# Performance work log

Hardware: AMD Instinct MI355X
Metric: run time of the kernel (lower is better)

Reference implementation:

```python
import jax, jax.numpy as jnp
import numpy as np


def _affine_mats(thetas, lambda1s, lambda2s, H, W):
    # Replicates torch.stack(rows, dim=1) then stack(dim=2): the 'rows' end up as COLUMNS,
    # exactly matching the original module's construction.
    z = jnp.zeros_like(lambda1s)
    o = jnp.ones_like(lambda1s)
    scale = jnp.stack([jnp.stack([lambda1s, z, z], 1),
                       jnp.stack([z, lambda2s, z], 1),
                       jnp.stack([z, z, o], 1)], axis=2)  # [B,3,3]
    th = -thetas
    rot = jnp.stack([jnp.stack([jnp.cos(th), jnp.sin(th), z], 1),
                     jnp.stack([-jnp.sin(th), jnp.cos(th), z], 1),
                     jnp.stack([z, z, o], 1)], axis=2)
    trans = jnp.stack([jnp.stack([o, z, o * W], 1),
                       jnp.stack([z, o, o * H], 1),
                       jnp.stack([z, z, o], 1)], axis=2)
    fw = rot @ trans                       # forward_warp
    fws = scale @ fw                       # forward_warp_scaled
    overall = jnp.linalg.inv(jnp.linalg.inv(fw) @ fws)
    return overall[:, 0:2, :]              # [B,2,3]


def _affine_grid(theta, H, W):
    # torch affine_grid, align_corners=False: normalized pixel-center coords in [-1,1]
    xs = (jnp.arange(W, dtype=theta.dtype) + 0.5) * (2.0 / W) - 1.0
    ys = (jnp.arange(H, dtype=theta.dtype) + 0.5) * (2.0 / H) - 1.0
    X, Y = jnp.meshgrid(xs, ys)                        # [H,W]
    base = jnp.stack([X, Y, jnp.ones_like(X)], -1)     # [H,W,3]
    return jnp.einsum('bij,hwj->bhwi', theta, base)    # [B,H,W,2] (x,y)


def _grid_sample_bilinear_zeros(x, grid):
    # torch grid_sample(mode='bilinear', padding_mode='zeros', align_corners=False)
    B, C, H, W = x.shape
    gx = (grid[..., 0] + 1.0) * (W * 0.5) - 0.5        # [B,H,W] source pixel coords
    gy = (grid[..., 1] + 1.0) * (H * 0.5) - 0.5
    x0 = jnp.floor(gx); y0 = jnp.floor(gy)
    x1 = x0 + 1.0;      y1 = y0 + 1.0
    wx1 = gx - x0; wx0 = 1.0 - wx1
    wy1 = gy - y0; wy0 = 1.0 - wy1
    x0i = x0.astype(jnp.int32); x1i = x1.astype(jnp.int32)
    y0i = y0.astype(jnp.int32); y1i = y1.astype(jnp.int32)
    b_idx = jnp.arange(B)[:, None, None]

    def gather(yi, xi):
        yc = jnp.clip(yi, 0, H - 1)
        xc = jnp.clip(xi, 0, W - 1)
        v = x[b_idx, :, yc, xc]                        # [B,H,W,C]
        m = ((yi >= 0) & (yi < H) & (xi >= 0) & (xi < W)).astype(x.dtype)
        return v * m[..., None]

    out = (gather(y0i, x0i) * (wy0 * wx0)[..., None]
           + gather(y0i, x1i) * (wy0 * wx1)[..., None]
           + gather(y1i, x0i) * (wy1 * wx0)[..., None]
           + gather(y1i, x1i) * (wy1 * wx1)[..., None])  # [B,H,W,C]
    return jnp.transpose(out, (0, 3, 1, 2))            # [B,C,H,W]


def setup_inputs() -> dict:
    key = jax.random.key(0)
    k1, k2, k3, k4 = jax.random.split(key, 4)
    B, C, H, W = 32, 3, 512, 512
    return {
        'x': jax.random.normal(k1, (B, C, H, W), dtype=jnp.float32),
        'thetas': jax.random.normal(k2, (B,), dtype=jnp.float32),
        'lambda1s': jax.random.uniform(k3, (B,), dtype=jnp.float32),
        'lambda2s': jax.random.uniform(k4, (B,), dtype=jnp.float32),
    }


def reference(x, thetas, lambda1s, lambda2s):
    H, W = x.shape[2], x.shape[3]
    theta = _affine_mats(thetas, lambda1s, lambda2s, H, W)   # [B,2,3]
    grid = _affine_grid(theta, H, W)                         # [B,H,W,2]
    return _grid_sample_bilinear_zeros(x, grid).astype(jnp.float32)
```

## Files before the change

### kernel.cpp

```cpp
#include <hip/hip_runtime.h>
#include <math.h>

constexpr int B = 32;
constexpr int C = 3;
constexpr int H = 512;
constexpr int W = 512;
constexpr int HW = H * W;

typedef unsigned int v2u __attribute__((ext_vector_type(2)));
typedef float        v2f __attribute__((ext_vector_type(2)));

static __device__ __forceinline__ v2f bload2(__amdgpu_buffer_rsrc_t r, int voff) {
    v2u u = __builtin_amdgcn_raw_buffer_load_b64(r, voff, 0, 0);
    return __builtin_bit_cast(v2f, u);
}

__global__ __launch_bounds__(256)
void warp_kernel(const float* __restrict__ x,
                 const float* __restrict__ thetas,
                 const float* __restrict__ l1s,
                 const float* __restrict__ l2s,
                 float* __restrict__ out) {
    const int b = blockIdx.y;

    __shared__ float sc[4];
    if (threadIdx.x == 0) {
        double th = -(double)thetas[b];
        double c = cos(th), s = sin(th);
        double a = 1.0 / (double)l1s[b];
        double d = 1.0 / (double)l2s[b];
        sc[0] = (float)(a * c * c + d * s * s);
        sc[1] = (float)(c * s * (d - a));
        sc[2] = sc[1];
        sc[3] = (float)(a * s * s + d * c * c);
    }
    __syncthreads();
    const float t00 = sc[0], t01 = sc[1], t10 = sc[2], t11 = sc[3];

    const int tid   = threadIdx.x;
    const int lane  = tid & 63;
    const int wv    = tid >> 6;
    const int h     = (blockIdx.x << 1) | (wv >> 1);
    const int wbase = (wv & 1) << 8;

    const float Y = ((float)h + 0.5f) * (2.0f / (float)H) - 1.0f;

    __amdgpu_buffer_rsrc_t rs[C];
    #pragma unroll
    for (int ch = 0; ch < C; ++ch) {
        rs[ch] = __builtin_amdgcn_make_buffer_rsrc(
            (void*)(x + (size_t)(b * C + ch) * HW), (short)0, HW * 4, 0x00020000);
    }

    int   voff0[4], voff1[4];
    float sw0[4], sw1[4], sw2[4], sw3[4];
    bool  any_valid = false;

    #pragma unroll
    for (int j = 0; j < 4; ++j) {
        const int w = wbase + (j << 6) + lane;
        const float X = ((float)w + 0.5f) * (2.0f / (float)W) - 1.0f;
        const float gx = (t00 * X + t01 * Y + 1.0f) * ((float)W * 0.5f) - 0.5f;
        const float gy = (t10 * X + t11 * Y + 1.0f) * ((float)H * 0.5f) - 0.5f;

        const float x0f = floorf(gx), y0f = floorf(gy);
        const float wx1 = gx - x0f, wx0 = 1.0f - wx1;
        const float wy1 = gy - y0f, wy0 = 1.0f - wy1;

        const int x0 = (int)x0f, y0 = (int)y0f;
        const int x1 = x0 + 1,  y1 = y0 + 1;

        const bool vx0 = ((unsigned)x0 < (unsigned)W);
        const bool vx1 = ((unsigned)x1 < (unsigned)W);
        const bool vy0 = ((unsigned)y0 < (unsigned)H);
        const bool vy1 = ((unsigned)y1 < (unsigned)H);
        const bool anyx = vx0 || vx1;
        any_valid = any_valid || ((vy0 || vy1) && anyx);

        const int xb   = min(max(x0, 0), W - 2);
        const bool xeq = (x0 == xb);

        const int yc0 = min(max(y0, -1), H);
        const int yc1 = min(max(y1, -1), H);
        voff0[j] = anyx ? (yc0 * W + xb) * 4 : -1;
        voff1[j] = anyx ? (yc1 * W + xb) * 4 : -1;

        const float m00 = (vy0 && vx0) ? 1.0f : 0.0f;
        const float m01 = (vy0 && vx1) ? 1.0f : 0.0f;
        const float m10 = (vy1 && vx0) ? 1.0f : 0.0f;
        const float m11 = (vy1 && vx1) ? 1.0f : 0.0f;
        const float w00 = wy0 * wx0 * m00, w01 = wy0 * wx1 * m01;
        const float w10 = wy1 * wx0 * m10, w11 = wy1 * wx1 * m11;

        sw0[j] = xeq ? w00 : w01;
        sw1[j] = xeq ? w01 : w00;
        sw2[j] = xeq ? w10 : w11;
        sw3[j] = xeq ? w11 : w10;
    }

    float r[C][4];
    #pragma unroll
    for (int ch = 0; ch < C; ++ch)
        #pragma unroll
        for (int j = 0; j < 4; ++j) r[ch][j] = 0.0f;

    if (any_valid) {
        #pragma unroll
        for (int j = 0; j < 4; ++j) {
            #pragma unroll
            for (int ch = 0; ch < C; ++ch) {
                const v2f v0 = bload2(rs[ch], voff0[j]);
                const v2f v1 = bload2(rs[ch], voff1[j]);
                r[ch][j] = v0.x * sw0[j] + v0.y * sw1[j]
                         + v1.x * sw2[j] + v1.y * sw3[j];
            }
        }
    }

    const size_t obase = (size_t)b * C * HW + (size_t)h * W + (size_t)wbase + lane;
    #pragma unroll
    for (int ch = 0; ch < C; ++ch) {
        #pragma unroll
        for (int j = 0; j < 4; ++j) {
            out[obase + (size_t)ch * HW + (j << 6)] = r[ch][j];
        }
    }
}

extern "C" void kernel_launch(void* const* d_in, const int* in_sizes, int n_in,
                              void* d_out, int out_size, void* d_ws, size_t ws_size,
                              hipStream_t stream) {
    const float* x      = (const float*)d_in[0];
    const float* thetas = (const float*)d_in[1];
    const float* l1s    = (const float*)d_in[2];
    const float* l2s    = (const float*)d_in[3];
    float* out          = (float*)d_out;

    warp_kernel<<<dim3(H / 2, B), 256, 0, stream>>>(x, thetas, l1s, l2s, out);
}
```

Baseline: 191.0 us.

## Pack input into interleaved fp16 workspace before bilinear warp gather

Adds a pre-pass that converts the three float32 channels into an interleaved half-precision layout with a padding channel, stored in workspace. The warp kernel then fetches all channels of two neighbouring pixels with one 128-bit buffer load per row, reducing the number of gather instructions. The cost is an extra full pass over the input plus a workspace write, and reduced input precision. It falls back to the original kernel when the workspace is too small.

```diff
diff --git a/kernel.cpp b/kernel.cpp
--- a/kernel.cpp
+++ b/kernel.cpp
@@ -1,4 +1,5 @@
 #include <hip/hip_runtime.h>
+#include <hip/hip_fp16.h>
 #include <math.h>
 
 constexpr int B = 32;
@@ -7,16 +8,53 @@
 constexpr int W = 512;
 constexpr int HW = H * W;
 
+typedef unsigned int v4u __attribute__((ext_vector_type(4)));
 typedef unsigned int v2u __attribute__((ext_vector_type(2)));
 typedef float        v2f __attribute__((ext_vector_type(2)));
 
+static __device__ __forceinline__ v4u bload4(__amdgpu_buffer_rsrc_t r, int voff) {
+    return __builtin_amdgcn_raw_buffer_load_b128(r, voff, 0, 0);
+}
 static __device__ __forceinline__ v2f bload2(__amdgpu_buffer_rsrc_t r, int voff) {
     v2u u = __builtin_amdgcn_raw_buffer_load_b64(r, voff, 0, 0);
     return __builtin_bit_cast(v2f, u);
 }
+static __device__ __forceinline__ float2 h2f2(unsigned int u) {
+    __half2 h = __builtin_bit_cast(__half2, u);
+    return __half22float2(h);
+}
+
 
 __global__ __launch_bounds__(256)
-void warp_kernel(const float* __restrict__ x,
+void pack_kernel(const float* __restrict__ x, __half* __restrict__ st) {
+    const int b  = blockIdx.y;
+    const int h  = (blockIdx.x << 1) | (threadIdx.x >> 7);
+    const int w4 = (threadIdx.x & 127) << 2;
+
+    const float* __restrict__ p0 = x + (size_t)(b * C + 0) * HW + h * W + w4;
+    const float* __restrict__ p1 = x + (size_t)(b * C + 1) * HW + h * W + w4;
+    const float* __restrict__ p2 = x + (size_t)(b * C + 2) * HW + h * W + w4;
+    const float4 a0 = *reinterpret_cast<const float4*>(p0);
+    const float4 a1 = *reinterpret_cast<const float4*>(p1);
+    const float4 a2 = *reinterpret_cast<const float4*>(p2);
+
+    union { __half h[16]; v4u u[2]; } pk;
+    pk.h[0]  = __float2half(a0.x); pk.h[1]  = __float2half(a1.x);
+    pk.h[2]  = __float2half(a2.x); pk.h[3]  = __half(0.0f);
+    pk.h[4]  = __float2half(a0.y); pk.h[5]  = __float2half(a1.y);
+    pk.h[6]  = __float2half(a2.y); pk.h[7]  = __half(0.0f);
+    pk.h[8]  = __float2half(a0.z); pk.h[9]  = __float2half(a1.z);
+    pk.h[10] = __float2half(a2.z); pk.h[11] = __half(0.0f);
+    pk.h[12] = __float2half(a0.w); pk.h[13] = __float2half(a1.w);
+    pk.h[14] = __float2half(a2.w); pk.h[15] = __half(0.0f);
+
+    __half* dst = st + ((size_t)b * HW + (size_t)h * W + w4) * 4;
+    reinterpret_cast<v4u*>(dst)[0] = pk.u[0];
+    reinterpret_cast<v4u*>(dst)[1] = pk.u[1];
+}
+
+__global__ __launch_bounds__(256)
+void warp_kernel(const __half* __restrict__ st,
                  const float* __restrict__ thetas,
                  const float* __restrict__ l1s,
                  const float* __restrict__ l2s,
@@ -45,12 +83,8 @@
 
     const float Y = ((float)h + 0.5f) * (2.0f / (float)H) - 1.0f;
 
-    __amdgpu_buffer_rsrc_t rs[C];
-    #pragma unroll
-    for (int ch = 0; ch < C; ++ch) {
-        rs[ch] = __builtin_amdgcn_make_buffer_rsrc(
-            (void*)(x + (size_t)(b * C + ch) * HW), (short)0, HW * 4, 0x00020000);
-    }
+    __amdgpu_buffer_rsrc_t rs = __builtin_amdgcn_make_buffer_rsrc(
+        (void*)(st + (size_t)b * HW * 4), (short)0, HW * 8, 0x00020000);
 
     int   voff0[4], voff1[4];
     float sw0[4], sw1[4], sw2[4], sw3[4];
@@ -82,8 +116,8 @@
 
         const int yc0 = min(max(y0, -1), H);
         const int yc1 = min(max(y1, -1), H);
-        voff0[j] = anyx ? (yc0 * W + xb) * 4 : -1;
-        voff1[j] = anyx ? (yc1 * W + xb) * 4 : -1;
+        voff0[j] = anyx ? (yc0 * W + xb) * 8 : -64;
+        voff1[j] = anyx ? (yc1 * W + xb) * 8 : -64;
 
         const float m00 = (vy0 && vx0) ? 1.0f : 0.0f;
         const float m01 = (vy0 && vx1) ? 1.0f : 0.0f;
@@ -98,33 +132,126 @@
         sw3[j] = xeq ? w11 : w10;
     }
 
+    float r0[4], r1[4], r2[4];
+    #pragma unroll
+    for (int j = 0; j < 4; ++j) { r0[j] = 0.0f; r1[j] = 0.0f; r2[j] = 0.0f; }
+
+    if (any_valid) {
+        #pragma unroll
+        for (int j = 0; j < 4; ++j) {
+            const v4u u0 = bload4(rs, voff0[j]);
+            const v4u u1 = bload4(rs, voff1[j]);
+            const float2 a01 = h2f2(u0.x); const float2 a2p = h2f2(u0.y);
+            const float2 b01 = h2f2(u0.z); const float2 b2p = h2f2(u0.w);
+            const float2 c01 = h2f2(u1.x); const float2 c2p = h2f2(u1.y);
+            const float2 d01 = h2f2(u1.z); const float2 d2p = h2f2(u1.w);
+            r0[j] = a01.x * sw0[j] + b01.x * sw1[j] + c01.x * sw2[j] + d01.x * sw3[j];
+            r1[j] = a01.y * sw0[j] + b01.y * sw1[j] + c01.y * sw2[j] + d01.y * sw3[j];
+            r2[j] = a2p.x * sw0[j] + b2p.x * sw1[j] + c2p.x * sw2[j] + d2p.x * sw3[j];
+        }
+    }
+
+    const size_t obase = (size_t)b * C * HW + (size_t)h * W + (size_t)wbase + lane;
+    #pragma unroll
+    for (int j = 0; j < 4; ++j) {
+        out[obase + 0 * (size_t)HW + (j << 6)] = r0[j];
+        out[obase + 1 * (size_t)HW + (j << 6)] = r1[j];
+        out[obase + 2 * (size_t)HW + (j << 6)] = r2[j];
+    }
+}
+
+__global__ __launch_bounds__(256)
+void warp_fallback(const float* __restrict__ x,
+                   const float* __restrict__ thetas,
+                   const float* __restrict__ l1s,
+                   const float* __restrict__ l2s,
+                   float* __restrict__ out) {
+    const int b = blockIdx.y;
+    __shared__ float sc[4];
+    if (threadIdx.x == 0) {
+        double th = -(double)thetas[b];
+        double c = cos(th), s = sin(th);
+        double a = 1.0 / (double)l1s[b];
+        double d = 1.0 / (double)l2s[b];
+        sc[0] = (float)(a * c * c + d * s * s);
+        sc[1] = (float)(c * s * (d - a));
+        sc[2] = sc[1];
+        sc[3] = (float)(a * s * s + d * c * c);
+    }
+    __syncthreads();
+    const float t00 = sc[0], t01 = sc[1], t10 = sc[2], t11 = sc[3];
+
+    const int tid   = threadIdx.x;
+    const int lane  = tid & 63;
+    const int wv    = tid >> 6;
+    const int h     = (blockIdx.x << 1) | (wv >> 1);
+    const int wbase = (wv & 1) << 8;
+    const float Y = ((float)h + 0.5f) * (2.0f / (float)H) - 1.0f;
+
+    __amdgpu_buffer_rsrc_t rs[C];
+    #pragma unroll
+    for (int ch = 0; ch < C; ++ch)
+        rs[ch] = __builtin_amdgcn_make_buffer_rsrc(
+            (void*)(x + (size_t)(b * C + ch) * HW), (short)0, HW * 4, 0x00020000);
+
+    int voff0[4], voff1[4];
+    float sw0[4], sw1[4], sw2[4], sw3[4];
+    bool any_valid = false;
+    #pragma unroll
+    for (int j = 0; j < 4; ++j) {
+        const int w = wbase + (j << 6) + lane;
+        const float X = ((float)w + 0.5f) * (2.0f / (float)W) - 1.0f;
+        const float gx = (t00 * X + t01 * Y + 1.0f) * ((float)W * 0.5f) - 0.5f;
+        const float gy = (t10 * X + t11 * Y + 1.0f) * ((float)H * 0.5f) - 0.5f;
+        const float x0f = floorf(gx), y0f = floorf(gy);
+        const float wx1 = gx - x0f, wx0 = 1.0f - wx1;
+        const float wy1 = gy - y0f, wy0 = 1.0f - wy1;
+        const int x0 = (int)x0f, y0 = (int)y0f;
+        const int x1 = x0 + 1,  y1 = y0 + 1;
+        const bool vx0 = ((unsigned)x0 < (unsigned)W);
+        const bool vx1 = ((unsigned)x1 < (unsigned)W);
+        const bool vy0 = ((unsigned)y0 < (unsigned)H);
+        const bool vy1 = ((unsigned)y1 < (unsigned)H);
+        const bool anyx = vx0 || vx1;
+        any_valid = any_valid || ((vy0 || vy1) && anyx);
+        const int xb = min(max(x0, 0), W - 2);
+        const bool xeq = (x0 == xb);
+        const int yc0 = min(max(y0, -1), H);
+        const int yc1 = min(max(y1, -1), H);
+        voff0[j] = anyx ? (yc0 * W + xb) * 4 : -1;
+        voff1[j] = anyx ? (yc1 * W + xb) * 4 : -1;
+        const float m00 = (vy0 && vx0) ? 1.0f : 0.0f;
+        const float m01 = (vy0 && vx1) ? 1.0f : 0.0f;
+        const float m10 = (vy1 && vx0) ? 1.0f : 0.0f;
+        const float m11 = (vy1 && vx1) ? 1.0f : 0.0f;
+        const float w00 = wy0 * wx0 * m00, w01 = wy0 * wx1 * m01;
+        const float w10 = wy1 * wx0 * m10, w11 = wy1 * wx1 * m11;
+        sw0[j] = xeq ? w00 : w01;
+        sw1[j] = xeq ? w01 : w00;
+        sw2[j] = xeq ? w10 : w11;
+        sw3[j] = xeq ? w11 : w10;
+    }
     float r[C][4];
     #pragma unroll
     for (int ch = 0; ch < C; ++ch)
         #pragma unroll
         for (int j = 0; j < 4; ++j) r[ch][j] = 0.0f;
-
     if (any_valid) {
         #pragma unroll
-        for (int j = 0; j < 4; ++j) {
+        for (int j = 0; j < 4; ++j)
             #pragma unroll
             for (int ch = 0; ch < C; ++ch) {
                 const v2f v0 = bload2(rs[ch], voff0[j]);
                 const v2f v1 = bload2(rs[ch], voff1[j]);
-                r[ch][j] = v0.x * sw0[j] + v0.y * sw1[j]
-                         + v1.x * sw2[j] + v1.y * sw3[j];
+                r[ch][j] = v0.x * sw0[j] + v0.y * sw1[j] + v1.x * sw2[j] + v1.y * sw3[j];
             }
-        }
-    }
-
+    }
     const size_t obase = (size_t)b * C * HW + (size_t)h * W + (size_t)wbase + lane;
     #pragma unroll
-    for (int ch = 0; ch < C; ++ch) {
-        #pragma unroll
-        for (int j = 0; j < 4; ++j) {
+    for (int ch = 0; ch < C; ++ch)
+        #pragma unroll
+        for (int j = 0; j < 4; ++j)
             out[obase + (size_t)ch * HW + (j << 6)] = r[ch][j];
-        }
-    }
 }
 
 extern "C" void kernel_launch(void* const* d_in, const int* in_sizes, int n_in,
@@ -136,5 +263,12 @@
     const float* l2s    = (const float*)d_in[3];
     float* out          = (float*)d_out;
 
-    warp_kernel<<<dim3(H / 2, B), 256, 0, stream>>>(x, thetas, l1s, l2s, out);
-}
+    const size_t need = (size_t)B * HW * 4 * sizeof(__half);
+    if (ws_size >= need) {
+        __half* st = (__half*)d_ws;
+        pack_kernel<<<dim3(H / 2, B), 256, 0, stream>>>(x, st);
+        warp_kernel<<<dim3(H / 2, B), 256, 0, stream>>>(st, thetas, l1s, l2s, out);
+    } else {
+        warp_fallback<<<dim3(H / 2, B), 256, 0, stream>>>(x, thetas, l1s, l2s, out);
+    }
+}
```

Measured after the change: 206.6 us. 8.1% more time.
